# Kernel optimization log

Measured on AMD Instinct MI355X. Metric: run time of the kernel, lower is better.

The kernel has to match this reference:

```python
import jax, jax.numpy as jnp
import numpy as np

B, N, D = 4, 1024, 1024
H, DH = 16, 64
N_LAYERS = 3  # len(mlp_dims) - 1 with implicit_mlp_hiddens=(64, 64)
EPS = 1.1920929e-07  # torch.nn.RMSNorm default eps = finfo(float32).eps


def _rope_tables(n, dtype):
    # lucidrains RotaryEmbedding: theta=10000, interleaved freq repeat
    inv_freq = 1.0 / (10000.0 ** (np.arange(0, DH, 2, dtype=np.float64) / DH))
    t = np.arange(n, dtype=np.float64)[:, None] * inv_freq[None, :]  # [n, DH/2]
    t = np.repeat(t, 2, axis=-1)  # [n, DH], freqs interleaved (f0,f0,f1,f1,...)
    return jnp.asarray(np.cos(t), dtype), jnp.asarray(np.sin(t), dtype)


def _rope_rotate(x, cos, sin):
    # x: [b,h,n,d]; rotate_half on interleaved pairs: (x1,x2) -> (-x2,x1)
    xp = x.reshape(*x.shape[:-1], DH // 2, 2)
    xr = jnp.stack((-xp[..., 1], xp[..., 0]), axis=-1).reshape(x.shape)
    return x * cos + xr * sin


def _attend(q, k, v):
    # rotate_queries_with_cached_keys with no cache: same positions for q and k
    n = q.shape[-2]
    cos, sin = _rope_tables(n, q.dtype)
    q = _rope_rotate(q, cos, sin)
    k = _rope_rotate(k, cos, sin)
    scale = DH ** -0.5
    scores = jnp.einsum('bhqd,bhkd->bhqk', q, k) * scale
    causal = jnp.tril(jnp.ones((n, n), dtype=bool))
    scores = jnp.where(causal, scores, -jnp.inf)
    attn = jax.nn.softmax(scores, axis=-1)
    return jnp.einsum('bhqk,bhkd->bhqd', attn, v)


def _split_heads(x):
    b, n, _ = x.shape
    return x.reshape(b, n, H, DH).transpose(0, 2, 1, 3)  # b h n d


def setup_inputs() -> dict:
    key = jax.random.key(0)
    ks = jax.random.split(key, 6)
    s = 0.02
    return {
        'tokens': jax.random.normal(ks[0], (B, N, D), jnp.float32),
        'gamma': jnp.ones((D,), jnp.float32),                                  # RMSNorm weight
        'Wq': jax.random.normal(ks[1], (D, H * DH), jnp.float32) * s,           # to_queries
        'Wk': jax.random.normal(ks[2], (N_LAYERS, D, H * DH), jnp.float32) * s, # stacked key projections
        'Wv': jax.random.normal(ks[3], (N_LAYERS, D, H * DH), jnp.float32) * s, # stacked value projections
        'Wo': jax.random.normal(ks[4], (H * DH, D), jnp.float32) * s,           # to_out
    }


def reference(tokens, gamma, Wq, Wk, Wv, Wo):
    b, n, d = tokens.shape
    # RMSNorm (prenorm)
    x = tokens * jax.lax.rsqrt(jnp.mean(tokens * tokens, axis=-1, keepdims=True) + EPS) * gamma
    out = _split_heads(x @ Wq)  # queries, [b h n d]
    for i in range(N_LAYERS):
        k = _split_heads(x @ Wk[i])
        v = _split_heads(x @ Wv[i])
        out = _attend(out, k, v)
        if i < N_LAYERS - 1:
            out = jax.nn.silu(out)  # implicit MLP activation between attention stages
    out = out.transpose(0, 2, 1, 3).reshape(b, n, H * DH)  # merge heads
    return out @ Wo
```

## Files before the change

kernel.cpp:

```cpp
#include <hip/hip_runtime.h>


typedef unsigned short u16;
typedef short s16x8 __attribute__((ext_vector_type(8)));
typedef u16 u16x4 __attribute__((ext_vector_type(4)));
typedef float f32x4 __attribute__((ext_vector_type(4)));

typedef __attribute__((address_space(1))) const unsigned int as1c_uint;
typedef __attribute__((address_space(3))) unsigned int as3_uint;

__device__ __forceinline__ float b2f(u16 h) {
  union { unsigned int u; float f; } v; v.u = ((unsigned int)h) << 16; return v.f;
}
__device__ __forceinline__ u16 f2b(float f) {
  union { float f; unsigned int u; } v; v.f = f;
  return (u16)((v.u + 0x7FFFu + ((v.u >> 16) & 1u)) >> 16);
}
__device__ __forceinline__ void gload16(const u16* g, const u16* lds) {
  __builtin_amdgcn_global_load_lds((as1c_uint*)(size_t)g,
                                   (as3_uint*)(unsigned int)(size_t)lds, 16, 0, 0);
}

__global__ __launch_bounds__(256)
void rmsnorm_kernel(const float* __restrict__ T, const float* __restrict__ gamma,
                    u16* __restrict__ X) {
  const int row = blockIdx.x, tid = threadIdx.x;
  const float4 v = ((const float4*)(T + (size_t)row * 1024))[tid];
  float ss = v.x * v.x + v.y * v.y + v.z * v.z + v.w * v.w;
#pragma unroll
  for (int msk = 1; msk <= 32; msk <<= 1) ss += __shfl_xor(ss, msk, 64);
  __shared__ float red[4];
  if ((tid & 63) == 0) red[tid >> 6] = ss;
  __syncthreads();
  const float tot = red[0] + red[1] + red[2] + red[3];
  const float r = rsqrtf(tot * (1.0f / 1024.0f) + 1.1920929e-07f);
  const float4 gm = ((const float4*)gamma)[tid];
  u16x4 o;
  o[0] = f2b(v.x * r * gm.x); o[1] = f2b(v.y * r * gm.y);
  o[2] = f2b(v.z * r * gm.z); o[3] = f2b(v.w * r * gm.w);
  *(u16x4*)(X + (size_t)row * 1024 + tid * 4) = o;
}

__global__ __launch_bounds__(256)
void rope_kernel(float* __restrict__ ct, float* __restrict__ st) {
  const int idx = blockIdx.x * 256 + threadIdx.x;
  const int n = idx >> 5, j = idx & 31;
  const double freq = pow(10000.0, -(double)j / 32.0);
  const double a = (double)n * freq;
  ct[idx] = (float)cos(a);
  st[idx] = (float)sin(a);
}

__global__ __launch_bounds__(256)
void transw_kernel(const float* __restrict__ Wq, const float* __restrict__ Wk,
                   const float* __restrict__ Wv, const float* __restrict__ Wo,
                   u16* __restrict__ wt) {
  __shared__ float tile[64][65];
  const int z = blockIdx.z;
  const float* src = (z == 0) ? Wq
                   : (z <= 3) ? (Wk + (size_t)(z - 1) * 1048576)
                   : (z <= 6) ? (Wv + (size_t)(z - 4) * 1048576)
                              : Wo;
  u16* dst = wt + (size_t)z * 1048576;
  const int tid = threadIdx.x;
  const int bx = blockIdx.x * 64;
  const int by = blockIdx.y * 64;
  const int tcol = (tid & 15) * 4, trow = tid >> 4;
#pragma unroll
  for (int i = 0; i < 4; ++i) {
    const int r = trow + i * 16;
    const float4 v = *(const float4*)(src + (size_t)(bx + r) * 1024 + by + tcol);
    tile[r][tcol] = v.x; tile[r][tcol + 1] = v.y;
    tile[r][tcol + 2] = v.z; tile[r][tcol + 3] = v.w;
  }
  __syncthreads();
  const int k4 = (tid & 15) * 4;
#pragma unroll
  for (int j = 0; j < 4; ++j) {
    const int R = (tid >> 4) + j * 16;
    u16x4 o;
    o[0] = f2b(tile[k4][R]);     o[1] = f2b(tile[k4 + 1][R]);
    o[2] = f2b(tile[k4 + 2][R]); o[3] = f2b(tile[k4 + 3][R]);
    *(u16x4*)&dst[(size_t)(by + R) * 1024 + bx + k4] = o;
  }
}

template <int KIND>
__global__ __launch_bounds__(256, 2)
void gemm_kernel(const u16* __restrict__ A, const u16* __restrict__ Bt,
                 void* __restrict__ Cout, const float* __restrict__ ct,
                 const float* __restrict__ st) {
  constexpr int MB = (KIND == 0) ? 8 : 4;
  constexpr int BM = MB * 32;
  constexpr int ASLOT = BM * 32;
  constexpr int SLOT = (BM + 128) * 32;
  const int p = blockIdx.x;
  const int role = (p & 7) * (KIND == 0 ? 112 : 64) + (p >> 3);
  const int z = (KIND == 0) ? (role >> 7) : (role >> 8);
  const int rem = (KIND == 0) ? (role & 127) : (role & 255);
  const int m0 = (rem >> 3) * BM;
  const int n0 = (rem & 7) * 128;

  const int tid = threadIdx.x;
  const int w = tid >> 6, l = tid & 63;
  const int g = l >> 4, ll = l & 15;
  const int wr = w >> 1, wc = w & 1;

  const u16* Ab;
  const u16* Bb;
  if (KIND == 0) {
    Ab = A + (size_t)m0 * 1024;
    Bb = Bt + (size_t)z * 1048576 + (size_t)n0 * 1024;
  } else {
    Ab = A + (size_t)m0 * 1024 + z * 512;
    Bb = Bt + (size_t)n0 * 1024 + z * 512;
  }

  __shared__ u16 SH[3][SLOT];

  const f32x4 zero = {0.f, 0.f, 0.f, 0.f};
  f32x4 acc[MB][4];
#pragma unroll
  for (int i = 0; i < MB; ++i)
#pragma unroll
    for (int j = 0; j < 4; ++j) acc[i][j] = zero;

  auto stage = [&](int t2) {
    const int slot = t2 % 3;
    const int k0 = t2 * 32;
    const int rsub = l >> 2, sl = l & 3;
#pragma unroll
    for (int c = 0; c < MB / 2; ++c) {
      const int chunk = c * 4 + w;
      const int row = chunk * 16 + rsub;
      const int kk = k0 + ((sl ^ ((row >> 1) & 3)) << 3);
      gload16(Ab + (size_t)row * 1024 + kk, &SH[slot][chunk * 512]);
    }
#pragma unroll
    for (int c = 0; c < 2; ++c) {
      const int chunk = c * 4 + w;
      const int row = chunk * 16 + rsub;
      const int kk = k0 + ((sl ^ ((row >> 1) & 3)) << 3);
      gload16(Bb + (size_t)row * 1024 + kk, &SH[slot][ASLOT + chunk * 512]);
    }
  };

  const int NT = (KIND == 1) ? 16 : 32;
  stage(0); stage(1);

#pragma unroll
  for (int t = 0; t < NT; ++t) {
    if (t < NT - 1) {
      if constexpr (KIND == 0) asm volatile("s_waitcnt vmcnt(6)" ::: "memory");
      else                     asm volatile("s_waitcnt vmcnt(4)" ::: "memory");
    } else {
      asm volatile("s_waitcnt vmcnt(0)" ::: "memory");
    }
    __builtin_amdgcn_s_barrier();

    const int slot = t % 3;
    const u16* As = &SH[slot][0];
    const u16* Bs = &SH[slot][ASLOT];
    s16x8 bfr[4];
#pragma unroll
    for (int nf = 0; nf < 4; ++nf) {
      const int row = wc * 64 + nf * 16 + ll;
      bfr[nf] = *(const s16x8*)&Bs[row * 32 + ((g ^ ((row >> 1) & 3)) << 3)];
    }
    s16x8 af[MB];
#pragma unroll
    for (int mf = 0; mf < MB; ++mf) {
      const int row = wr * (MB * 16) + mf * 16 + ll;
      af[mf] = *(const s16x8*)&As[row * 32 + ((g ^ ((row >> 1) & 3)) << 3)];
    }

    if (t + 2 < NT) stage(t + 2);

    __builtin_amdgcn_s_setprio(1);
#pragma unroll
    for (int mf = 0; mf < MB; ++mf)
#pragma unroll
      for (int nf = 0; nf < 4; ++nf)
        acc[mf][nf] = __builtin_amdgcn_mfma_f32_16x16x32_bf16(af[mf], bfr[nf],
                                                              acc[mf][nf], 0, 0, 0);
    __builtin_amdgcn_s_setprio(0);
  }
  __syncthreads();

  if (KIND == 0) {
    u16* C = (u16*)Cout + (size_t)z * 4194304;
    if (z < 4) {
      const bool doRope = (z >= 1);
      u16* T = &SH[0][0];
#pragma unroll
      for (int mf = 0; mf < MB; ++mf)
#pragma unroll
        for (int nf = 0; nf < 4; ++nf) {
          const int c = wc * 64 + nf * 16 + ll;
#pragma unroll
          for (int rg = 0; rg < 4; ++rg) {
            const int r = wr * (MB * 16) + mf * 16 + g * 4 + rg;
            T[r * 128 + (c ^ ((r & 7) << 4))] = f2b(acc[mf][nf][rg]);
          }
        }
      __syncthreads();
#pragma unroll
      for (int i = 0; i < BM / 16; ++i) {
        const int R = (tid >> 4) + i * 16;
        const int c0 = (tid & 15) * 8;
        s16x8 v = *(const s16x8*)&T[R * 128 + (c0 ^ ((R & 7) << 4))];
        if (doRope) {
          const int n = (m0 + R) & 1023;
          const int j0 = (c0 & 63) >> 1;
          const float4 c4 = *(const float4*)(ct + n * 32 + j0);
          const float4 s4 = *(const float4*)(st + n * 32 + j0);
          s16x8 vo;
#pragma unroll
          for (int pp = 0; pp < 4; ++pp) {
            const float c = ((const float*)&c4)[pp];
            const float s = ((const float*)&s4)[pp];
            const float x0 = b2f((u16)v[2 * pp]), x1 = b2f((u16)v[2 * pp + 1]);
            vo[2 * pp]     = (short)f2b(x0 * c - x1 * s);
            vo[2 * pp + 1] = (short)f2b(x1 * c + x0 * s);
          }
          v = vo;
        }
        *(s16x8*)&C[(size_t)(m0 + R) * 1024 + n0 + c0] = v;
      }
    } else {
#pragma unroll
      for (int mf = 0; mf < MB; ++mf)
#pragma unroll
        for (int nf = 0; nf < 4; ++nf) {
          const int col = n0 + wc * 64 + nf * 16 + ll;
          const int hh = col >> 6, d = col & 63;
          const int mb = m0 + wr * (MB * 16) + mf * 16 + g * 4;
          const int bb = mb >> 10, n = mb & 1023;
          u16x4 pk;
#pragma unroll
          for (int rg = 0; rg < 4; ++rg) pk[rg] = f2b(acc[mf][nf][rg]);
          *(u16x4*)&C[((size_t)((bb * 16 + hh) * 64 + d)) * 1024 + n] = pk;
        }
    }
  } else {
    float* C = (float*)Cout + (size_t)z * 4194304;
#pragma unroll
    for (int mf = 0; mf < MB; ++mf)
#pragma unroll
      for (int nf = 0; nf < 4; ++nf) {
        const int col = n0 + wc * 64 + nf * 16 + ll;
#pragma unroll
        for (int rg = 0; rg < 4; ++rg) {
          const int m = m0 + wr * (MB * 16) + mf * 16 + g * 4 + rg;
          C[(size_t)m * 1024 + col] = acc[mf][nf][rg];
        }
      }
  }
}

__global__ __launch_bounds__(256)
void reduce_kernel(const float* __restrict__ P, float* __restrict__ out) {
  const int i = (blockIdx.x * 256 + threadIdx.x) * 4;
  const float4 a = *(const float4*)(P + i);
  const float4 b = *(const float4*)(P + 4194304 + i);
  float4 o;
  o.x = a.x + b.x; o.y = a.y + b.y; o.z = a.z + b.z; o.w = a.w + b.w;
  *(float4*)(out + i) = o;
}

template <int SILU>
__global__ __launch_bounds__(256)
void attn_kernel(const u16* __restrict__ Q, const u16* __restrict__ K,
                 const u16* __restrict__ Vt, u16* __restrict__ O,
                 const float* __restrict__ ct, const float* __restrict__ st) {
  const int lin = blockIdx.x + (blockIdx.y << 3);
  const int role = (lin & 7) * 64 + (lin >> 3);
  const int p = role & 7, bh = role >> 3;
  const int q_lo = p, q_hi = 15 - p;
  const int b = bh >> 4, h = bh & 15;
  const int tid = threadIdx.x, w = tid >> 6, l = tid & 63;
  const int g = l >> 4, ll = l & 15;

  const u16* Qb = Q + (size_t)(b * 1024) * 1024 + h * 64;
  const u16* Kb = K + (size_t)(b * 1024) * 1024 + h * 64;
  const u16* Vb = Vt + (size_t)((b * 16 + h) * 64) * 1024;
  u16* Ob = O + (size_t)(b * 1024) * 1024 + h * 64;

  __shared__ u16 Ksh[2][128 * 72];
  __shared__ u16 Psh[4][16 * 72];

  s16x8 qfL[2], qfH[2];
  auto loadQ = [&](int qt, s16x8* qf) {
    const int qrow = qt * 64 + w * 16 + ll;
#pragma unroll
    for (int kc = 0; kc < 2; ++kc) {
      const int d0 = kc * 32 + g * 8;
      const int j0 = d0 >> 1;
      const float4 c4 = *(const float4*)(ct + qrow * 32 + j0);
      const float4 s4v = *(const float4*)(st + qrow * 32 + j0);
      const s16x8 qin = *(const s16x8*)(Qb + (size_t)qrow * 1024 + d0);
      s16x8 qo;
#pragma unroll
      for (int pp = 0; pp < 4; ++pp) {
        const float c = ((const float*)&c4)[pp], s = ((const float*)&s4v)[pp];
        const float x0 = b2f((u16)qin[2 * pp]), x1 = b2f((u16)qin[2 * pp + 1]);
        qo[2 * pp]     = (short)f2b((x0 * c - x1 * s) * 0.125f);
        qo[2 * pp + 1] = (short)f2b((x1 * c + x0 * s) * 0.125f);
      }
      qf[kc] = qo;
    }
  };
  loadQ(q_lo, qfL);
  loadQ(q_hi, qfH);

  float lsL[4], lsH[4];
  f32x4 oL[4], oH[4];
  const f32x4 zero = {0.f, 0.f, 0.f, 0.f};
#pragma unroll
  for (int rg = 0; rg < 4; ++rg) { lsL[rg] = 0.f; lsH[rg] = 0.f; }
#pragma unroll
  for (int df = 0; df < 4; ++df) { oL[df] = zero; oH[df] = zero; }

  const int srow = tid >> 2;
  const int sc0 = (tid & 3) * 16;

  s16x8 kr0, kr1, kr2, kr3;
  auto kload = [&](int tt) {
    const u16* kp = Kb + (size_t)(tt * 128 + srow) * 1024 + sc0;
    kr0 = *(const s16x8*)kp;
    kr1 = *(const s16x8*)(kp + 8);
    const u16* kp2 = kp + (size_t)64 * 1024;
    kr2 = *(const s16x8*)kp2;
    kr3 = *(const s16x8*)(kp2 + 8);
  };
  auto kstore = [&](int bf) {
    *(s16x8*)&Ksh[bf][srow * 72 + sc0] = kr0;
    *(s16x8*)&Ksh[bf][srow * 72 + sc0 + 8] = kr1;
    *(s16x8*)&Ksh[bf][(64 + srow) * 72 + sc0] = kr2;
    *(s16x8*)&Ksh[bf][(64 + srow) * 72 + sc0 + 8] = kr3;
  };

  kload(0);
  kstore(0);
  __syncthreads();
  int buf = 0;

  const int iters = (q_hi + 2) >> 1;
  for (int tt = 0; tt < iters; ++tt) {
    const bool pre = (tt + 1 < iters);
    if (pre) kload(tt + 1);

    s16x8 vb[2][2][4];
#pragma unroll
    for (int sub = 0; sub < 2; ++sub)
#pragma unroll
      for (int kc = 0; kc < 2; ++kc)
#pragma unroll
        for (int df = 0; df < 4; ++df)
          vb[sub][kc][df] = *(const s16x8*)(Vb + (size_t)(df * 16 + ll) * 1024 +
                                           (tt * 2 + sub) * 64 + kc * 32 + g * 8);

    auto process = [&](const s16x8* qf, float* ls, f32x4* o, int sub,
                       bool diag) {
      const int rb = sub * 64;
      f32x4 s4[4];
      __builtin_amdgcn_s_setprio(1);
#pragma unroll
      for (int nf = 0; nf < 4; ++nf) {
        const s16x8 kb0 = *(const s16x8*)&Ksh[buf][(rb + nf * 16 + ll) * 72 + g * 8];
        const s16x8 kb1 = *(const s16x8*)&Ksh[buf][(rb + nf * 16 + ll) * 72 + 32 + g * 8];
        f32x4 sv = zero;
        sv = __builtin_amdgcn_mfma_f32_16x16x32_bf16(qf[0], kb0, sv, 0, 0, 0);
        sv = __builtin_amdgcn_mfma_f32_16x16x32_bf16(qf[1], kb1, sv, 0, 0, 0);
        s4[nf] = sv;
      }
      __builtin_amdgcn_s_setprio(0);

      if (diag) {
#pragma unroll
        for (int nf = 0; nf < 4; ++nf)
#pragma unroll
          for (int rg = 0; rg < 4; ++rg)
            if (nf * 16 + ll > w * 16 + g * 4 + rg) s4[nf][rg] = -3.0e38f;
      }

#pragma unroll
      for (int rg = 0; rg < 4; ++rg) {
        float ps = 0.f;
#pragma unroll
        for (int nf = 0; nf < 4; ++nf) {
          const float pv = __expf(s4[nf][rg] - 12.f);
          s4[nf][rg] = pv;
          ps += pv;
        }
        ls[rg] += ps;
      }

#pragma unroll
      for (int nf = 0; nf < 4; ++nf)
#pragma unroll
        for (int rg = 0; rg < 4; ++rg)
          Psh[w][(g * 4 + rg) * 72 + nf * 16 + ll] = f2b(s4[nf][rg]);

      __builtin_amdgcn_s_setprio(1);
#pragma unroll
      for (int kc = 0; kc < 2; ++kc) {
        const s16x8 pa = *(const s16x8*)&Psh[w][ll * 72 + kc * 32 + g * 8];
#pragma unroll
        for (int df = 0; df < 4; ++df)
          o[df] = __builtin_amdgcn_mfma_f32_16x16x32_bf16(pa, vb[sub][kc][df],
                                                          o[df], 0, 0, 0);
      }
      __builtin_amdgcn_s_setprio(0);
    };

    const int ka = 2 * tt, kb = 2 * tt + 1;
    process(qfH, lsH, oH, 0, ka == q_hi);
    if (kb <= q_hi) process(qfH, lsH, oH, 1, kb == q_hi);
    if (ka <= q_lo) process(qfL, lsL, oL, 0, ka == q_lo);
    if (kb <= q_lo) process(qfL, lsL, oL, 1, kb == q_lo);

    if (pre) kstore(buf ^ 1);
    __syncthreads();
    buf ^= 1;
  }

  auto finish = [&](float* ls, f32x4* o, int qt) {
#pragma unroll
    for (int rg = 0; rg < 4; ++rg) {
      float v = ls[rg];
      v += __shfl_xor(v, 1, 64);
      v += __shfl_xor(v, 2, 64);
      v += __shfl_xor(v, 4, 64);
      v += __shfl_xor(v, 8, 64);
      ls[rg] = 1.f / v;
    }
#pragma unroll
    for (int df = 0; df < 4; ++df)
#pragma unroll
      for (int rg = 0; rg < 4; ++rg) {
        float val = o[df][rg] * ls[rg];
        if (SILU) val = val / (1.f + __expf(-val));
        Ob[(size_t)(qt * 64 + w * 16 + g * 4 + rg) * 1024 + df * 16 + ll] =
            f2b(val);
      }
  };
  finish(lsH, oH, q_hi);
  finish(lsL, oL, q_lo);
}

extern "C" void kernel_launch(void* const* d_in, const int* in_sizes, int n_in,
                              void* d_out, int out_size, void* d_ws, size_t ws_size,
                              hipStream_t stream) {
  (void)in_sizes; (void)n_in; (void)out_size; (void)ws_size;
  const float* tokens = (const float*)d_in[0];
  const float* gamma  = (const float*)d_in[1];
  const float* Wq     = (const float*)d_in[2];
  const float* Wk     = (const float*)d_in[3];
  const float* Wv     = (const float*)d_in[4];
  const float* Wo     = (const float*)d_in[5];
  float* out = (float*)d_out;

  u16* x    = (u16*)d_ws;
  u16* wt   = x + (size_t)4096 * 1024;
  u16* qkv  = wt + (size_t)8 * 1048576;
  u16* outA = qkv + (size_t)7 * 4194304;
  u16* outB = outA + 4194304;
  float* ct = (float*)(outB + 4194304);
  float* st = ct + 32768;
  float* Pp = (float*)(qkv + 1 * 4194304);

  rmsnorm_kernel<<<4096, 256, 0, stream>>>(tokens, gamma, x);
  rope_kernel<<<128, 256, 0, stream>>>(ct, st);
  transw_kernel<<<dim3(16, 16, 8), 256, 0, stream>>>(Wq, Wk, Wv, Wo, wt);
  gemm_kernel<0><<<896, 256, 0, stream>>>(x, wt, qkv, ct, st);

  const size_t M4 = 4194304;
  attn_kernel<1><<<dim3(8, 64), 256, 0, stream>>>(qkv, qkv + 1 * M4, qkv + 4 * M4,
                                                  outA, ct, st);
  attn_kernel<1><<<dim3(8, 64), 256, 0, stream>>>(outA, qkv + 2 * M4, qkv + 5 * M4,
                                                  outB, ct, st);
  attn_kernel<0><<<dim3(8, 64), 256, 0, stream>>>(outB, qkv + 3 * M4, qkv + 6 * M4,
                                                  outA, ct, st);

  gemm_kernel<1><<<512, 256, 0, stream>>>(outA, wt + (size_t)7 * 1048576,
                                          (void*)Pp, ct, st);
  reduce_kernel<<<4096, 256, 0, stream>>>(Pp, out);
}
```

Before: 228.8 us.

## Merge prep kernels and cut attention register pressure for higher occupancy

```diff
diff --git a/kernel.cpp b/kernel.cpp
--- a/kernel.cpp
+++ b/kernel.cpp
@@ -22,66 +22,63 @@
 }
 
 __global__ __launch_bounds__(256)
-void rmsnorm_kernel(const float* __restrict__ T, const float* __restrict__ gamma,
-                    u16* __restrict__ X) {
-  const int row = blockIdx.x, tid = threadIdx.x;
-  const float4 v = ((const float4*)(T + (size_t)row * 1024))[tid];
-  float ss = v.x * v.x + v.y * v.y + v.z * v.z + v.w * v.w;
-#pragma unroll
-  for (int msk = 1; msk <= 32; msk <<= 1) ss += __shfl_xor(ss, msk, 64);
-  __shared__ float red[4];
-  if ((tid & 63) == 0) red[tid >> 6] = ss;
-  __syncthreads();
-  const float tot = red[0] + red[1] + red[2] + red[3];
-  const float r = rsqrtf(tot * (1.0f / 1024.0f) + 1.1920929e-07f);
-  const float4 gm = ((const float4*)gamma)[tid];
-  u16x4 o;
-  o[0] = f2b(v.x * r * gm.x); o[1] = f2b(v.y * r * gm.y);
-  o[2] = f2b(v.z * r * gm.z); o[3] = f2b(v.w * r * gm.w);
-  *(u16x4*)(X + (size_t)row * 1024 + tid * 4) = o;
-}
-
-__global__ __launch_bounds__(256)
-void rope_kernel(float* __restrict__ ct, float* __restrict__ st) {
-  const int idx = blockIdx.x * 256 + threadIdx.x;
-  const int n = idx >> 5, j = idx & 31;
-  const double freq = pow(10000.0, -(double)j / 32.0);
-  const double a = (double)n * freq;
-  ct[idx] = (float)cos(a);
-  st[idx] = (float)sin(a);
-}
-
-__global__ __launch_bounds__(256)
-void transw_kernel(const float* __restrict__ Wq, const float* __restrict__ Wk,
-                   const float* __restrict__ Wv, const float* __restrict__ Wo,
-                   u16* __restrict__ wt) {
-  __shared__ float tile[64][65];
-  const int z = blockIdx.z;
-  const float* src = (z == 0) ? Wq
-                   : (z <= 3) ? (Wk + (size_t)(z - 1) * 1048576)
-                   : (z <= 6) ? (Wv + (size_t)(z - 4) * 1048576)
-                              : Wo;
-  u16* dst = wt + (size_t)z * 1048576;
-  const int tid = threadIdx.x;
-  const int bx = blockIdx.x * 64;
-  const int by = blockIdx.y * 64;
-  const int tcol = (tid & 15) * 4, trow = tid >> 4;
-#pragma unroll
-  for (int i = 0; i < 4; ++i) {
-    const int r = trow + i * 16;
-    const float4 v = *(const float4*)(src + (size_t)(bx + r) * 1024 + by + tcol);
-    tile[r][tcol] = v.x; tile[r][tcol + 1] = v.y;
-    tile[r][tcol + 2] = v.z; tile[r][tcol + 3] = v.w;
-  }
-  __syncthreads();
-  const int k4 = (tid & 15) * 4;
-#pragma unroll
-  for (int j = 0; j < 4; ++j) {
-    const int R = (tid >> 4) + j * 16;
+void prep_kernel(const float* __restrict__ T, const float* __restrict__ gamma,
+                 u16* __restrict__ X, float* __restrict__ ct,
+                 float* __restrict__ st, const float* __restrict__ Wq,
+                 const float* __restrict__ Wk, const float* __restrict__ Wv,
+                 const float* __restrict__ Wo, u16* __restrict__ wt) {
+  __shared__ float shbuf[64 * 65];
+  const int bid = blockIdx.x, tid = threadIdx.x;
+  if (bid < 4096) {
+    const int row = bid;
+    const float4 v = ((const float4*)(T + (size_t)row * 1024))[tid];
+    float ss = v.x * v.x + v.y * v.y + v.z * v.z + v.w * v.w;
+#pragma unroll
+    for (int msk = 1; msk <= 32; msk <<= 1) ss += __shfl_xor(ss, msk, 64);
+    if ((tid & 63) == 0) shbuf[tid >> 6] = ss;
+    __syncthreads();
+    const float tot = shbuf[0] + shbuf[1] + shbuf[2] + shbuf[3];
+    const float r = rsqrtf(tot * (1.0f / 1024.0f) + 1.1920929e-07f);
+    const float4 gm = ((const float4*)gamma)[tid];
     u16x4 o;
-    o[0] = f2b(tile[k4][R]);     o[1] = f2b(tile[k4 + 1][R]);
-    o[2] = f2b(tile[k4 + 2][R]); o[3] = f2b(tile[k4 + 3][R]);
-    *(u16x4*)&dst[(size_t)(by + R) * 1024 + bx + k4] = o;
+    o[0] = f2b(v.x * r * gm.x); o[1] = f2b(v.y * r * gm.y);
+    o[2] = f2b(v.z * r * gm.z); o[3] = f2b(v.w * r * gm.w);
+    *(u16x4*)(X + (size_t)row * 1024 + tid * 4) = o;
+  } else if (bid < 4224) {
+    const int idx = (bid - 4096) * 256 + tid;
+    const int n = idx >> 5, j = idx & 31;
+    const double freq = pow(10000.0, -(double)j / 32.0);
+    const double a = (double)n * freq;
+    ct[idx] = (float)cos(a);
+    st[idx] = (float)sin(a);
+  } else {
+    const int t = bid - 4224;
+    const int z = t >> 8, rem = t & 255;
+    const float* src = (z == 0) ? Wq
+                     : (z <= 3) ? (Wk + (size_t)(z - 1) * 1048576)
+                     : (z <= 6) ? (Wv + (size_t)(z - 4) * 1048576)
+                                : Wo;
+    u16* dst = wt + (size_t)z * 1048576;
+    const int bx = (rem & 15) * 64;
+    const int by = (rem >> 4) * 64;
+    const int tcol = (tid & 15) * 4, trow = tid >> 4;
+#pragma unroll
+    for (int i = 0; i < 4; ++i) {
+      const int r = trow + i * 16;
+      const float4 v = *(const float4*)(src + (size_t)(bx + r) * 1024 + by + tcol);
+      shbuf[r * 65 + tcol] = v.x; shbuf[r * 65 + tcol + 1] = v.y;
+      shbuf[r * 65 + tcol + 2] = v.z; shbuf[r * 65 + tcol + 3] = v.w;
+    }
+    __syncthreads();
+    const int k4 = (tid & 15) * 4;
+#pragma unroll
+    for (int j2 = 0; j2 < 4; ++j2) {
+      const int R = (tid >> 4) + j2 * 16;
+      u16x4 o;
+      o[0] = f2b(shbuf[k4 * 65 + R]);       o[1] = f2b(shbuf[(k4 + 1) * 65 + R]);
+      o[2] = f2b(shbuf[(k4 + 2) * 65 + R]); o[3] = f2b(shbuf[(k4 + 3) * 65 + R]);
+      *(u16x4*)&dst[(size_t)(by + R) * 1024 + bx + k4] = o;
+    }
   }
 }
 
@@ -269,7 +266,7 @@
 }
 
 template <int SILU>
-__global__ __launch_bounds__(256)
+__global__ __launch_bounds__(256, 3)
 void attn_kernel(const u16* __restrict__ Q, const u16* __restrict__ K,
                  const u16* __restrict__ Vt, u16* __restrict__ O,
                  const float* __restrict__ ct, const float* __restrict__ st) {
@@ -350,19 +347,17 @@
     const bool pre = (tt + 1 < iters);
     if (pre) kload(tt + 1);
 
-    s16x8 vb[2][2][4];
-#pragma unroll
-    for (int sub = 0; sub < 2; ++sub)
-#pragma unroll
-      for (int kc = 0; kc < 2; ++kc)
-#pragma unroll
-        for (int df = 0; df < 4; ++df)
-          vb[sub][kc][df] = *(const s16x8*)(Vb + (size_t)(df * 16 + ll) * 1024 +
-                                           (tt * 2 + sub) * 64 + kc * 32 + g * 8);
-
     auto process = [&](const s16x8* qf, float* ls, f32x4* o, int sub,
                        bool diag) {
       const int rb = sub * 64;
+      s16x8 vbs[2][4];
+#pragma unroll
+      for (int kc = 0; kc < 2; ++kc)
+#pragma unroll
+        for (int df = 0; df < 4; ++df)
+          vbs[kc][df] = *(const s16x8*)(Vb + (size_t)(df * 16 + ll) * 1024 +
+                                        (tt * 2 + sub) * 64 + kc * 32 + g * 8);
+
       f32x4 s4[4];
       __builtin_amdgcn_s_setprio(1);
 #pragma unroll
@@ -408,17 +403,17 @@
         const s16x8 pa = *(const s16x8*)&Psh[w][ll * 72 + kc * 32 + g * 8];
 #pragma unroll
         for (int df = 0; df < 4; ++df)
-          o[df] = __builtin_amdgcn_mfma_f32_16x16x32_bf16(pa, vb[sub][kc][df],
+          o[df] = __builtin_amdgcn_mfma_f32_16x16x32_bf16(pa, vbs[kc][df],
                                                           o[df], 0, 0, 0);
       }
       __builtin_amdgcn_s_setprio(0);
     };
 
-    const int ka = 2 * tt, kb = 2 * tt + 1;
+    const int ka = 2 * tt, kb2 = 2 * tt + 1;
     process(qfH, lsH, oH, 0, ka == q_hi);
-    if (kb <= q_hi) process(qfH, lsH, oH, 1, kb == q_hi);
+    if (kb2 <= q_hi) process(qfH, lsH, oH, 1, kb2 == q_hi);
     if (ka <= q_lo) process(qfL, lsL, oL, 0, ka == q_lo);
-    if (kb <= q_lo) process(qfL, lsL, oL, 1, kb == q_lo);
+    if (kb2 <= q_lo) process(qfL, lsL, oL, 1, kb2 == q_lo);
 
     if (pre) kstore(buf ^ 1);
     __syncthreads();
@@ -470,9 +465,8 @@
   float* st = ct + 32768;
   float* Pp = (float*)(qkv + 1 * 4194304);
 
-  rmsnorm_kernel<<<4096, 256, 0, stream>>>(tokens, gamma, x);
-  rope_kernel<<<128, 256, 0, stream>>>(ct, st);
-  transw_kernel<<<dim3(16, 16, 8), 256, 0, stream>>>(Wq, Wk, Wv, Wo, wt);
+  prep_kernel<<<6272, 256, 0, stream>>>(tokens, gamma, x, ct, st,
+                                        Wq, Wk, Wv, Wo, wt);
   gemm_kernel<0><<<896, 256, 0, stream>>>(x, wt, qkv, ct, st);
 
   const size_t M4 = 4194304;
```

Result: slower. 233.6 us (+2.1%).
